# Performance work log

Hardware: AMD Instinct MI355X
Metric: run time of the kernel (lower is better)

## Reference

```python
import jax, jax.numpy as jnp
import numpy as np

DIM = 2048
STATE = 2048
SEL_H = 1024
B = 16384


def setup_inputs() -> dict:
    key = jax.random.key(0)
    ks = jax.random.split(key, 7)
    def lin(k, out_f, in_f):
        return jax.random.normal(k, (out_f, in_f), dtype=jnp.float32) / np.sqrt(in_f)
    return {
        "x_t": jax.random.normal(ks[0], (B, DIM), dtype=jnp.float32),
        "h_prev": jax.random.normal(ks[1], (B, STATE), dtype=jnp.float32),
        "W_in": lin(ks[2], STATE, DIM),
        "W_sel_in": lin(ks[3], SEL_H, DIM),
        "W_sel_out": lin(ks[4], 4 * STATE, SEL_H),
        "W_out": lin(ks[5], DIM, STATE),
        "d": jnp.ones((STATE,), dtype=jnp.float32),
    }


def reference(x_t, h_prev, W_in, W_sel_in, W_sel_out, W_out, d):
    # u_t = in_proj(x_t): [B, state]
    u_t = x_t @ W_in.T
    # selector: silu(x @ W_sel_in.T) @ W_sel_out.T -> [B, 4*state]
    sel_h = jax.nn.silu(x_t @ W_sel_in.T)
    sel = sel_h @ W_sel_out.T
    a_raw, b_raw, c_raw, d_raw = jnp.split(sel, 4, axis=-1)
    a_t = jax.nn.sigmoid(a_raw)
    b_t = jnp.tanh(b_raw)
    c_t = jnp.tanh(c_raw)
    d_t = jax.nn.sigmoid(d_raw)
    h_t = a_t * h_prev + b_t * u_t
    y_t = c_t * h_t + d[None, :] * d_t * u_t
    out = y_t @ W_out.T  # [B, dim]
    return (out, h_t)
```

## Files before the change

kernel.cpp:

```cpp
#include <hip/hip_runtime.h>
#include <hip/hip_bf16.h>
#include <cstdint>

#define NB    16384
#define DIMX  2048
#define STATE 2048
#define SELH  1024

typedef unsigned short u16;
typedef short  short8_t __attribute__((ext_vector_type(8)));
typedef float  f32x4    __attribute__((ext_vector_type(4)));

__device__ __forceinline__ u16 f2bf(float f) {
  unsigned u = __builtin_bit_cast(unsigned, f);
  u += 0x7fffu + ((u >> 16) & 1u);
  return (u16)(u >> 16);
}
__device__ __forceinline__ float bf2f(u16 h) {
  unsigned u = ((unsigned)h) << 16;
  return __builtin_bit_cast(float, u);
}
__device__ __forceinline__ float sigmoidf_(float x) { return 1.f / (1.f + __expf(-x)); }
__device__ __forceinline__ float tanhf_(float x)    { return 2.f / (1.f + __expf(-2.f * x)) - 1.f; }

__device__ __forceinline__ f32x4 mfma_bf16(short8_t a, short8_t b, f32x4 c) {
  return __builtin_amdgcn_mfma_f32_16x16x32_bf16(a, b, c, 0, 0, 0);
}

__device__ __forceinline__ void gload16(const void* g, const void* l) {
  __builtin_amdgcn_global_load_lds(
      (const __attribute__((address_space(1))) unsigned int*)(uintptr_t)g,
      (__attribute__((address_space(3))) unsigned int*)(unsigned int)(uintptr_t)l,
      16, 0, 0);
}

#define LDS_V(p) (*(const short8_t*)__builtin_assume_aligned((const void*)(p), 16))

__global__ __launch_bounds__(256) void k_convert5(const float* __restrict__ s0, u16* __restrict__ d0, int n0,
                                                  const float* __restrict__ s1, u16* __restrict__ d1, int n1,
                                                  const float* __restrict__ s2, u16* __restrict__ d2, int n2,
                                                  const float* __restrict__ s3, u16* __restrict__ d3, int n3,
                                                  const float* __restrict__ s4, u16* __restrict__ d4, int n4) {
  const int base = blockIdx.x * blockDim.x + threadIdx.x;
  const int stride = gridDim.x * blockDim.x;
#define SEG(S, D, N)                                                     \
  for (int i = base; i < (N); i += stride) {                             \
    float4 v = ((const float4*)(S))[i];                                  \
    ushort4 o;                                                           \
    o.x = f2bf(v.x); o.y = f2bf(v.y); o.z = f2bf(v.z); o.w = f2bf(v.w);  \
    ((ushort4*)(D))[i] = o;                                              \
  }
  SEG(s0, d0, n0) SEG(s1, d1, n1) SEG(s2, d2, n2) SEG(s3, d3, n3) SEG(s4, d4, n4)
#undef SEG
}

template <int EPI, int KD, int NCOLS>
__global__ __launch_bounds__(512, 2) void k_gemm256(const u16* __restrict__ A,
                                                    const u16* __restrict__ Bsrc,
                                                    float* __restrict__ f32out,
                                                    u16* __restrict__ bfout,
                                                    const float* __restrict__ hprev,
                                                    const u16* __restrict__ ubf,
                                                    const float* __restrict__ dvec,
                                                    u16* __restrict__ bfout2) {
  __shared__ __align__(16) char smem[131072];
  const int tid = threadIdx.x;
  const int w = tid >> 6, l = tid & 63;
  const int wr = w >> 2, wc = w & 3;
  const int bx = blockIdx.x, by = blockIdx.y;
  const int m0 = by * 256;

  const unsigned aAddr0 = (unsigned)(wr * 16384 + (l & 15) * 128 +
                                     (((l >> 4) * 16) ^ ((l & 7) << 4)));
  const unsigned aAddr1 = aAddr0 ^ 64u;
  const unsigned bAddr0 = (unsigned)(65536 + (wc * 64 + (l & 15)) * 64 +
                                     (((l >> 4) * 16) ^ ((l & 3) << 4)));
  const unsigned bAddr1 = bAddr0 + 16384u;

  const int rA = tid >> 3;
  const int kA = ((tid & 7) ^ ((tid >> 3) & 7)) * 8;
  const u16* aSrc = A + (size_t)(m0 + rA) * KD + kA;

  const int rB = tid >> 2;
  const int kB = ((tid & 3) ^ ((tid >> 2) & 3)) * 8;
  size_t bRow0, bRow1;
  if constexpr (EPI != 3) {
    bRow0 = (size_t)bx * 256 + rB;
    bRow1 = bRow0 + 128;
  } else {
    const int s0 = bx * 64;
    const int r1 = rB + 128;
    bRow0 = (size_t)((rB >> 4) & 3) * STATE + s0 + (rB >> 6) * 16 + (rB & 15);
    bRow1 = (size_t)((r1 >> 4) & 3) * STATE + s0 + (r1 >> 6) * 16 + (r1 & 15);
  }
  const u16* bSrc0 = Bsrc + bRow0 * KD + kB;
  const u16* bSrc1 = Bsrc + bRow1 * KD + kB;

  auto stageA = [&](int k0n, int rh, unsigned dstD) {
    const u16* sp = aSrc + (size_t)rh * 128 * KD + k0n;
    gload16(sp,           smem + dstD + (unsigned)rh * 16384u + (unsigned)tid * 16u);
    gload16(sp + 64 * KD, smem + dstD + (unsigned)rh * 16384u + 8192u + (unsigned)tid * 16u);
  };
  auto stageB = [&](int k0n, int kh, unsigned dstD) {
    const int kk = k0n + kh * 32;
    gload16(bSrc0 + kk, smem + 65536u + dstD + (unsigned)kh * 16384u + (unsigned)tid * 16u);
    gload16(bSrc1 + kk, smem + 65536u + dstD + (unsigned)kh * 16384u + 8192u + (unsigned)tid * 16u);
  };

  const unsigned hpBase = (w < 4) ? (unsigned)w * 8192u
                                  : 65536u + (unsigned)(w - 4) * 8192u;
  auto prefetchHP = [&]() {
    if constexpr (EPI == 3) {
      const float* hb = hprev + (size_t)(m0 + wr * 128 + (l >> 2)) * STATE +
                        bx * 64 + wc * 16 + (l & 3) * 4;
#pragma unroll
      for (int inst = 0; inst < 8; ++inst)
        gload16(hb + (size_t)inst * 16 * STATE,
                smem + hpBase + (unsigned)inst * 1024u + (unsigned)l * 16u);
    }
  };

  f32x4 acc[8][4];
#pragma unroll
  for (int i = 0; i < 8; ++i)
#pragma unroll
    for (int j = 0; j < 4; ++j) acc[i][j] = f32x4{0.f, 0.f, 0.f, 0.f};

  short8_t ava[8], avb[8], bv01a[2], bv23a[2], bv23b[2], bv01b[2];

#define KTILE(D, DO_STAGE, K0N, LASTT)                                         \
  {                                                                            \
                                                        \
    if (LASTT) { asm volatile("s_waitcnt vmcnt(0)" ::: "memory"); }            \
    else       { asm volatile("s_waitcnt vmcnt(2)" ::: "memory"); }            \
    __builtin_amdgcn_s_barrier();                                              \
    __builtin_amdgcn_sched_barrier(0);                                         \
    if (LASTT) prefetchHP();                                                   \
    bv01a[0] = LDS_V(smem + bAddr0 + (D) * 32768u);                            \
    bv01a[1] = LDS_V(smem + bAddr0 + (D) * 32768u + 1024u);                    \
    _Pragma("unroll") for (int mf = 0; mf < 8; ++mf)                           \
        ava[mf] = LDS_V(smem + aAddr0 + (D) * 32768u + mf * 2048u);            \
    if (DO_STAGE) { stageA(K0N, 0, (D ^ 1) * 32768u);                          \
                    stageA(K0N, 1, (D ^ 1) * 32768u); }                        \
    __builtin_amdgcn_s_setprio(1);                                             \
    _Pragma("unroll") for (int mf = 0; mf < 8; ++mf) {                         \
      acc[mf][0] = mfma_bf16(ava[mf], bv01a[0], acc[mf][0]);                   \
      acc[mf][1] = mfma_bf16(ava[mf], bv01a[1], acc[mf][1]);                   \
    }                                                                          \
    __builtin_amdgcn_s_setprio(0);                                             \
                                                                       \
    if (!LASTT) { asm volatile("s_waitcnt vmcnt(4)" ::: "memory"); }           \
    __builtin_amdgcn_s_barrier();                                              \
    __builtin_amdgcn_sched_barrier(0);                                         \
    bv23a[0] = LDS_V(smem + bAddr0 + (D) * 32768u + 2048u);                    \
    bv23a[1] = LDS_V(smem + bAddr0 + (D) * 32768u + 3072u);                    \
    bv23b[0] = LDS_V(smem + bAddr1 + (D) * 32768u + 2048u);                    \
    bv23b[1] = LDS_V(smem + bAddr1 + (D) * 32768u + 3072u);                    \
    _Pragma("unroll") for (int mf = 0; mf < 8; ++mf)                           \
        avb[mf] = LDS_V(smem + aAddr1 + (D) * 32768u + mf * 2048u);            \
    if (DO_STAGE) { stageB(K0N, 0, (D ^ 1) * 32768u);                          \
                    stageB(K0N, 1, (D ^ 1) * 32768u); }                        \
    __builtin_amdgcn_s_setprio(1);                                             \
    _Pragma("unroll") for (int mf = 0; mf < 8; ++mf) {                         \
      acc[mf][2] = mfma_bf16(ava[mf], bv23a[0], acc[mf][2]);                   \
      acc[mf][3] = mfma_bf16(ava[mf], bv23a[1], acc[mf][3]);                   \
    }                                                                          \
    __builtin_amdgcn_s_setprio(0);                                             \
                                                          \
    bv01b[0] = LDS_V(smem + bAddr1 + (D) * 32768u);                            \
    bv01b[1] = LDS_V(smem + bAddr1 + (D) * 32768u + 1024u);                    \
    __builtin_amdgcn_s_setprio(1);                                             \
    _Pragma("unroll") for (int mf = 0; mf < 8; ++mf) {                         \
      acc[mf][2] = mfma_bf16(avb[mf], bv23b[0], acc[mf][2]);                   \
      acc[mf][3] = mfma_bf16(avb[mf], bv23b[1], acc[mf][3]);                   \
    }                                                                          \
    __builtin_amdgcn_s_setprio(0);                                             \
                                                          \
    __builtin_amdgcn_s_setprio(1);                                             \
    _Pragma("unroll") for (int mf = 0; mf < 8; ++mf) {                         \
      acc[mf][0] = mfma_bf16(avb[mf], bv01b[0], acc[mf][0]);                   \
      acc[mf][1] = mfma_bf16(avb[mf], bv01b[1], acc[mf][1]);                   \
    }                                                                          \
    __builtin_amdgcn_s_setprio(0);                                             \
  }

  stageA(0, 0, 0u); stageA(0, 1, 0u); stageB(0, 0, 0u); stageB(0, 1, 0u);

  constexpr int NT = KD / 64;
  int k0 = 0;
#pragma unroll 1
  for (int T = 0; T < NT - 2; T += 2) {
    KTILE(0, true, k0 + 64, false);
    KTILE(1, true, k0 + 128, false);
    k0 += 128;
  }
  KTILE(0, true, k0 + 64, false);
  KTILE(1, false, 0, true);

#undef KTILE

  const int rbase = m0 + wr * 128 + ((l >> 4) << 2);
  if constexpr (EPI == 2) {
    const int cbase = bx * 256 + wc * 64 + (l & 15);
#pragma unroll
    for (int mf = 0; mf < 8; ++mf)
#pragma unroll
      for (int nf = 0; nf < 4; ++nf)
#pragma unroll
        for (int r = 0; r < 4; ++r) {
          const int row = rbase + mf * 16 + r;
          const int col = cbase + nf * 16;
          f32out[(size_t)row * NCOLS + col] = acc[mf][nf][r];
        }
  } else if constexpr (EPI == 5) {
    const int cbase = bx * 256 + wc * 64 + (l & 15);
    if (bx < STATE / 256) {
#pragma unroll
      for (int mf = 0; mf < 8; ++mf)
#pragma unroll
        for (int nf = 0; nf < 4; ++nf)
#pragma unroll
          for (int r = 0; r < 4; ++r) {
            const int row = rbase + mf * 16 + r;
            const int col = cbase + nf * 16;
            bfout[(size_t)row * STATE + col] = f2bf(acc[mf][nf][r]);
          }
    } else {
#pragma unroll
      for (int mf = 0; mf < 8; ++mf)
#pragma unroll
        for (int nf = 0; nf < 4; ++nf)
#pragma unroll
          for (int r = 0; r < 4; ++r) {
            const int row = rbase + mf * 16 + r;
            const int col = cbase + nf * 16 - STATE;
            const float v = acc[mf][nf][r];
            bfout2[(size_t)row * SELH + col] = f2bf(v * sigmoidf_(v));
          }
    }
  } else {
    asm volatile("s_waitcnt vmcnt(0)" ::: "memory");
    const int s = bx * 64 + wc * 16 + (l & 15);
    const float dval = dvec[s];
    const int lr0 = (l >> 4) << 2;
    u16 uuArr[8][4];
#pragma unroll
    for (int mf = 0; mf < 8; ++mf)
#pragma unroll
      for (int r = 0; r < 4; ++r)
        uuArr[mf][r] = ubf[(size_t)(rbase + mf * 16 + r) * STATE + s];
#pragma unroll
    for (int mf = 0; mf < 8; ++mf)
#pragma unroll
      for (int r = 0; r < 4; ++r) {
        const int row = rbase + mf * 16 + r;
        const size_t idx = (size_t)row * STATE + s;
        const float a  = acc[mf][0][r];
        const float b  = acc[mf][1][r];
        const float c  = acc[mf][2][r];
        const float dd = acc[mf][3][r];
        const float uu = bf2f(uuArr[mf][r]);
        const float hp = *(const float*)(smem + hpBase +
                          (unsigned)(mf * 16 + lr0 + r) * 64u +
                          (unsigned)(l & 15) * 4u);
        const float h = sigmoidf_(a) * hp + tanhf_(b) * uu;
        f32out[idx] = h;
        bfout[idx] = f2bf(tanhf_(c) * h + dval * sigmoidf_(dd) * uu);
      }
  }
}

extern "C" void kernel_launch(void* const* d_in, const int* in_sizes, int n_in,
                              void* d_out, int out_size, void* d_ws, size_t ws_size,
                              hipStream_t stream) {
  const float* x   = (const float*)d_in[0];
  const float* h0  = (const float*)d_in[1];
  const float* Win = (const float*)d_in[2];
  const float* Wsi = (const float*)d_in[3];
  const float* Wso = (const float*)d_in[4];
  const float* Wou = (const float*)d_in[5];
  const float* dv  = (const float*)d_in[6];
  float* out  = (float*)d_out;
  float* hout = out + (size_t)NB * DIMX;

  u16* ws = (u16*)d_ws;
  size_t o = 0;
  u16* xb   = ws + o; o += (size_t)NB * DIMX;
  u16* ub   = ws + o; o += (size_t)NB * STATE;
  u16* yb   = ws + o; o += (size_t)NB * STATE;
  u16* sh   = ws + o; o += (size_t)NB * SELH;
  u16* wib  = ws + o; o += (size_t)STATE * DIMX;
  u16* wsib = ws + o; o += (size_t)SELH * DIMX;
  u16* wsob = ws + o; o += (size_t)4 * STATE * SELH;
  u16* wob  = ws + o; o += (size_t)DIMX * STATE;

  k_convert5<<<2048, 256, 0, stream>>>(x,   xb,   NB * DIMX / 4,
                                       Win, wib,  STATE * DIMX / 4,
                                       Wsi, wsib, SELH * DIMX / 4,
                                       Wso, wsob, 4 * STATE * SELH / 4,
                                       Wou, wob,  DIMX * STATE / 4);

  const dim3 blk(512);
  k_gemm256<5, DIMX, 0><<<dim3((STATE + SELH) / 256, NB / 256), blk, 0, stream>>>(
      xb, wib, nullptr, ub, nullptr, nullptr, nullptr, sh);
  k_gemm256<3, SELH, 0><<<dim3(STATE / 64, NB / 256), blk, 0, stream>>>(
      sh, wsob, hout, yb, h0, ub, dv, nullptr);
  k_gemm256<2, STATE, DIMX><<<dim3(DIMX / 256, NB / 256), blk, 0, stream>>>(
      yb, wob, out, nullptr, nullptr, nullptr, nullptr, nullptr);
}
```

Baseline: 689.7 us.

## Load B operand fragments directly from global into registers, bypassing LDS

The B (weight) tile is no longer staged through shared memory. Each lane loads its MFMA B fragments straight from global memory into a double-buffered register set (Be/Bo), and only A keeps using global_load_lds double buffering. The K-tile loop is simplified to one full wait and barrier per tile, and the hprev prefetch region moves to the freed upper half of LDS. This cuts LDS traffic and barriers for B, but raises register pressure, uses uncoalesced 16-byte global reads with cross-wave redundancy, and drains vmcnt fully every tile, which removes some of the earlier overlap.

```diff
diff --git a/kernel.cpp b/kernel.cpp
--- a/kernel.cpp
+++ b/kernel.cpp
@@ -35,6 +35,7 @@
 }
 
 #define LDS_V(p) (*(const short8_t*)__builtin_assume_aligned((const void*)(p), 16))
+#define GLB_V(p) (*(const short8_t*)__builtin_assume_aligned((const void*)(p), 16))
 
 __global__ __launch_bounds__(256) void k_convert5(const float* __restrict__ s0, u16* __restrict__ d0, int n0,
                                                   const float* __restrict__ s1, u16* __restrict__ d1, int n1,
@@ -73,42 +74,35 @@
   const unsigned aAddr0 = (unsigned)(wr * 16384 + (l & 15) * 128 +
                                      (((l >> 4) * 16) ^ ((l & 7) << 4)));
   const unsigned aAddr1 = aAddr0 ^ 64u;
-  const unsigned bAddr0 = (unsigned)(65536 + (wc * 64 + (l & 15)) * 64 +
-                                     (((l >> 4) * 16) ^ ((l & 3) << 4)));
-  const unsigned bAddr1 = bAddr0 + 16384u;
 
   const int rA = tid >> 3;
   const int kA = ((tid & 7) ^ ((tid >> 3) & 7)) * 8;
   const u16* aSrc = A + (size_t)(m0 + rA) * KD + kA;
-
-  const int rB = tid >> 2;
-  const int kB = ((tid & 3) ^ ((tid >> 2) & 3)) * 8;
-  size_t bRow0, bRow1;
-  if constexpr (EPI != 3) {
-    bRow0 = (size_t)bx * 256 + rB;
-    bRow1 = bRow0 + 128;
-  } else {
-    const int s0 = bx * 64;
-    const int r1 = rB + 128;
-    bRow0 = (size_t)((rB >> 4) & 3) * STATE + s0 + (rB >> 6) * 16 + (rB & 15);
-    bRow1 = (size_t)((r1 >> 4) & 3) * STATE + s0 + (r1 >> 6) * 16 + (r1 & 15);
-  }
-  const u16* bSrc0 = Bsrc + bRow0 * KD + kB;
-  const u16* bSrc1 = Bsrc + bRow1 * KD + kB;
 
   auto stageA = [&](int k0n, int rh, unsigned dstD) {
     const u16* sp = aSrc + (size_t)rh * 128 * KD + k0n;
     gload16(sp,           smem + dstD + (unsigned)rh * 16384u + (unsigned)tid * 16u);
     gload16(sp + 64 * KD, smem + dstD + (unsigned)rh * 16384u + 8192u + (unsigned)tid * 16u);
   };
-  auto stageB = [&](int k0n, int kh, unsigned dstD) {
-    const int kk = k0n + kh * 32;
-    gload16(bSrc0 + kk, smem + 65536u + dstD + (unsigned)kh * 16384u + (unsigned)tid * 16u);
-    gload16(bSrc1 + kk, smem + 65536u + dstD + (unsigned)kh * 16384u + 8192u + (unsigned)tid * 16u);
-  };
-
-  const unsigned hpBase = (w < 4) ? (unsigned)w * 8192u
-                                  : 65536u + (unsigned)(w - 4) * 8192u;
+
+  const u16* bBase[4];
+#pragma unroll
+  for (int nf = 0; nf < 4; ++nf) {
+    size_t row;
+    if constexpr (EPI != 3) {
+      row = (size_t)bx * 256 + wc * 64 + nf * 16 + (l & 15);
+    } else {
+      row = (size_t)nf * STATE + bx * 64 + wc * 16 + (l & 15);
+    }
+    bBase[nf] = Bsrc + row * KD + ((l >> 4) * 8);
+  }
+
+#define LOADB(BARR, K0N)                                                       \
+  _Pragma("unroll") for (int kh = 0; kh < 2; ++kh)                             \
+    _Pragma("unroll") for (int nf = 0; nf < 4; ++nf)                           \
+        BARR[kh * 4 + nf] = GLB_V(bBase[nf] + (K0N) + kh * 32);
+
+  const unsigned hpBase = 65536u + (unsigned)w * 8192u;
   auto prefetchHP = [&]() {
     if constexpr (EPI == 3) {
       const float* hb = hprev + (size_t)(m0 + wr * 128 + (l >> 2)) * STATE +
@@ -126,78 +120,46 @@
 #pragma unroll
     for (int j = 0; j < 4; ++j) acc[i][j] = f32x4{0.f, 0.f, 0.f, 0.f};
 
-  short8_t ava[8], avb[8], bv01a[2], bv23a[2], bv23b[2], bv01b[2];
-
-#define KTILE(D, DO_STAGE, K0N, LASTT)                                         \
+  short8_t Be[8], Bo[8];
+
+#define TILE(DOFF, BCUR, BNXT, K0N, DO_NEXT, ISLAST)                           \
   {                                                                            \
-                                                        \
-    if (LASTT) { asm volatile("s_waitcnt vmcnt(0)" ::: "memory"); }            \
-    else       { asm volatile("s_waitcnt vmcnt(2)" ::: "memory"); }            \
+    asm volatile("s_waitcnt lgkmcnt(0)" ::: "memory");                         \
+    asm volatile("s_waitcnt vmcnt(0)" ::: "memory");                           \
     __builtin_amdgcn_s_barrier();                                              \
     __builtin_amdgcn_sched_barrier(0);                                         \
-    if (LASTT) prefetchHP();                                                   \
-    bv01a[0] = LDS_V(smem + bAddr0 + (D) * 32768u);                            \
-    bv01a[1] = LDS_V(smem + bAddr0 + (D) * 32768u + 1024u);                    \
-    _Pragma("unroll") for (int mf = 0; mf < 8; ++mf)                           \
-        ava[mf] = LDS_V(smem + aAddr0 + (D) * 32768u + mf * 2048u);            \
-    if (DO_STAGE) { stageA(K0N, 0, (D ^ 1) * 32768u);                          \
-                    stageA(K0N, 1, (D ^ 1) * 32768u); }                        \
-    __builtin_amdgcn_s_setprio(1);                                             \
-    _Pragma("unroll") for (int mf = 0; mf < 8; ++mf) {                         \
-      acc[mf][0] = mfma_bf16(ava[mf], bv01a[0], acc[mf][0]);                   \
-      acc[mf][1] = mfma_bf16(ava[mf], bv01a[1], acc[mf][1]);                   \
+    if (DO_NEXT) {                                                             \
+      stageA((K0N), 0, (DOFF) ^ 32768u);                                       \
+      stageA((K0N), 1, (DOFF) ^ 32768u);                                       \
+      LOADB(BNXT, (K0N));                                                      \
     }                                                                          \
-    __builtin_amdgcn_s_setprio(0);                                             \
-                                                                       \
-    if (!LASTT) { asm volatile("s_waitcnt vmcnt(4)" ::: "memory"); }           \
-    __builtin_amdgcn_s_barrier();                                              \
-    __builtin_amdgcn_sched_barrier(0);                                         \
-    bv23a[0] = LDS_V(smem + bAddr0 + (D) * 32768u + 2048u);                    \
-    bv23a[1] = LDS_V(smem + bAddr0 + (D) * 32768u + 3072u);                    \
-    bv23b[0] = LDS_V(smem + bAddr1 + (D) * 32768u + 2048u);                    \
-    bv23b[1] = LDS_V(smem + bAddr1 + (D) * 32768u + 3072u);                    \
-    _Pragma("unroll") for (int mf = 0; mf < 8; ++mf)                           \
-        avb[mf] = LDS_V(smem + aAddr1 + (D) * 32768u + mf * 2048u);            \
-    if (DO_STAGE) { stageB(K0N, 0, (D ^ 1) * 32768u);                          \
-                    stageB(K0N, 1, (D ^ 1) * 32768u); }                        \
-    __builtin_amdgcn_s_setprio(1);                                             \
-    _Pragma("unroll") for (int mf = 0; mf < 8; ++mf) {                         \
-      acc[mf][2] = mfma_bf16(ava[mf], bv23a[0], acc[mf][2]);                   \
-      acc[mf][3] = mfma_bf16(ava[mf], bv23a[1], acc[mf][3]);                   \
-    }                                                                          \
-    __builtin_amdgcn_s_setprio(0);                                             \
-                                                          \
-    bv01b[0] = LDS_V(smem + bAddr1 + (D) * 32768u);                            \
-    bv01b[1] = LDS_V(smem + bAddr1 + (D) * 32768u + 1024u);                    \
-    __builtin_amdgcn_s_setprio(1);                                             \
-    _Pragma("unroll") for (int mf = 0; mf < 8; ++mf) {                         \
-      acc[mf][2] = mfma_bf16(avb[mf], bv23b[0], acc[mf][2]);                   \
-      acc[mf][3] = mfma_bf16(avb[mf], bv23b[1], acc[mf][3]);                   \
-    }                                                                          \
-    __builtin_amdgcn_s_setprio(0);                                             \
-                                                          \
-    __builtin_amdgcn_s_setprio(1);                                             \
-    _Pragma("unroll") for (int mf = 0; mf < 8; ++mf) {                         \
-      acc[mf][0] = mfma_bf16(avb[mf], bv01b[0], acc[mf][0]);                   \
-      acc[mf][1] = mfma_bf16(avb[mf], bv01b[1], acc[mf][1]);                   \
-    }                                                                          \
-    __builtin_amdgcn_s_setprio(0);                                             \
-  }
-
-  stageA(0, 0, 0u); stageA(0, 1, 0u); stageB(0, 0, 0u); stageB(0, 1, 0u);
+    if (ISLAST) prefetchHP();                                                  \
+    _Pragma("unroll") for (int kh = 0; kh < 2; ++kh)                           \
+      _Pragma("unroll") for (int hf = 0; hf < 2; ++hf) {                       \
+        short8_t av[4];                                                        \
+        _Pragma("unroll") for (int mf = 0; mf < 4; ++mf)                       \
+            av[mf] = LDS_V(smem + (DOFF) + (kh ? aAddr1 : aAddr0) +            \
+                           (hf * 4 + mf) * 2048u);                             \
+        __builtin_amdgcn_s_setprio(1);                                         \
+        _Pragma("unroll") for (int mf = 0; mf < 4; ++mf)                       \
+          _Pragma("unroll") for (int nf = 0; nf < 4; ++nf)                     \
+              acc[hf * 4 + mf][nf] =                                           \
+                  mfma_bf16(av[mf], BCUR[kh * 4 + nf], acc[hf * 4 + mf][nf]);  \
+        __builtin_amdgcn_s_setprio(0);                                         \
+      }                                                                        \
+  }
+
+  stageA(0, 0, 0u); stageA(0, 1, 0u);
+  LOADB(Be, 0);
 
   constexpr int NT = KD / 64;
-  int k0 = 0;
 #pragma unroll 1
-  for (int T = 0; T < NT - 2; T += 2) {
-    KTILE(0, true, k0 + 64, false);
-    KTILE(1, true, k0 + 128, false);
-    k0 += 128;
-  }
-  KTILE(0, true, k0 + 64, false);
-  KTILE(1, false, 0, true);
-
-#undef KTILE
+  for (int T = 0; T < NT; T += 2) {
+    TILE(0u,     Be, Bo, (T + 1) * 64, (T + 1) < NT, false);
+    TILE(32768u, Bo, Be, (T + 2) * 64, (T + 2) < NT, (T + 2) >= NT);
+  }
+#undef TILE
+#undef LOADB
 
   const int rbase = m0 + wr * 128 + ((l >> 4) << 2);
   if constexpr (EPI == 2) {
```

Result: slower. 1.720 ms (+149.3%).
